# Kernel tuning notes

Hardware: AMD Instinct MI355X
Metric: run time of the kernel (lower is better)

## Reference

```python
import jax, jax.numpy as jnp
import numpy as np

N_NODES = 150000       # original nodes
N_FRAG_NODES = 300000  # nodes duplicated across fragments
N_FRAGS = 30000        # number of fragments (segments of fragments_batch)
E = 1200000            # edges in combined fragment graph
D = 128                # nhid


def seg_mean(x, seg, num):
    s = jax.ops.segment_sum(x, seg, num_segments=num)
    c = jax.ops.segment_sum(jnp.ones((x.shape[0], 1), x.dtype), seg, num_segments=num)
    return s / jnp.maximum(c, 1.0)


def setup_inputs() -> dict:
    key = jax.random.key(0)
    ks = jax.random.split(key, 8)
    x = jax.random.normal(ks[0], (N_NODES, D), dtype=jnp.float32)
    mapper = jax.random.randint(ks[1], (N_FRAG_NODES,), 0, N_NODES)
    batch = jnp.sort(jax.random.randint(ks[2], (N_FRAG_NODES,), 0, N_FRAGS))
    edge_index = jax.random.randint(ks[3], (2, E), 0, N_FRAG_NODES)
    W_u = jax.random.normal(ks[4], (D, D), dtype=jnp.float32) * 0.05
    b_u = jnp.zeros((D,), dtype=jnp.float32)
    W_gcn = jax.random.normal(ks[5], (D, D), dtype=jnp.float32) * 0.05
    b_gcn = jnp.zeros((D,), dtype=jnp.float32)
    return {
        "x": x,
        "fragments_nodes_mapper": mapper,
        "fragments_batch": batch,
        "edge_index": edge_index,
        "W_u": W_u,
        "b_u": b_u,
        "W_gcn": W_gcn,
        "b_gcn": b_gcn,
        "i": 0,
    }


def gcn_conv(x, edge_index, W, b, n):
    # PyG GCNConv: add self loops, symmetric normalization D^-1/2 (A+I) D^-1/2, then linear.
    xw = x @ W  # [n, D]
    loops = jnp.arange(n, dtype=edge_index.dtype)
    row = jnp.concatenate([edge_index[0], loops])  # source
    col = jnp.concatenate([edge_index[1], loops])  # target (aggregation index)
    deg = jax.ops.segment_sum(jnp.ones(row.shape[0], x.dtype), col, num_segments=n)
    dinv = jnp.where(deg > 0, jax.lax.rsqrt(jnp.maximum(deg, 1.0)), 0.0)
    norm = dinv[row] * dinv[col]  # [E+n]
    msg = xw[row] * norm[:, None]
    out = jax.ops.segment_sum(msg, col, num_segments=n)
    return out + b


def reference(x, fragments_nodes_mapper, fragments_batch, edge_index, W_u, b_u, W_gcn, b_gcn, i):
    if i == 0:
        x = x[fragments_nodes_mapper]  # gather: [N_FRAG_NODES, D]
    # fragment-level mean pooling, broadcast back to fragment-nodes
    fragment = seg_mean(x, fragments_batch, N_FRAGS)[fragments_batch]
    # U[i-1]: MLP(nhid, nhid, nlayer=1, with_final_activation=True) -> Linear + ReLU
    x = x + jax.nn.relu(fragment @ W_u + b_u)
    # pool duplicated fragment-nodes back onto original nodes, then re-broadcast
    x = seg_mean(x, fragments_nodes_mapper, N_NODES)[fragments_nodes_mapper]
    # GCN over the combined fragment graph
    x = gcn_conv(x, edge_index, W_gcn, b_gcn, N_FRAG_NODES)
    fragment_x = seg_mean(x, fragments_batch, N_FRAGS)  # [N_FRAGS, D]
    return (fragment_x, x)
```

## Files before the change

### kernel.cpp

```cpp
#include <hip/hip_runtime.h>
#include <hip/hip_bf16.h>

#define N_NODES      150000
#define N_FRAG_NODES 300000
#define N_FRAGS      30000
#define NEDGE        1200000
#define NCNT         (N_NODES + N_FRAG_NODES)
#define D            128
#define DV           32
#define SCAN_TILE    1024

typedef __attribute__((ext_vector_type(8))) short short8;
typedef __attribute__((ext_vector_type(8))) unsigned short u16x8;
typedef __attribute__((ext_vector_type(4))) float f32x4;
typedef __attribute__((ext_vector_type(2))) int i32x2;

__device__ __forceinline__ unsigned short f2bf(float f) {
    unsigned u = __float_as_uint(f);
    u = (u + 0x7FFFu + ((u >> 16) & 1u)) >> 16;
    return (unsigned short)u;
}
__device__ __forceinline__ float bf2f(unsigned short u) {
    return __uint_as_float((unsigned)u << 16);
}

__global__ void k_prep(const int* __restrict__ mapper, const int* __restrict__ batch,
                       const int* __restrict__ ecol, int* __restrict__ mcnt,
                       int* __restrict__ ccnt, int* __restrict__ startb) {
    int i = blockIdx.x * blockDim.x + threadIdx.x;
    if (i < NEDGE) atomicAdd(&ccnt[ecol[i]], 1);
    if (i < N_FRAG_NODES) atomicAdd(&mcnt[mapper[i]], 1);
    if (i <= N_FRAGS) {
        int lo = 0, hi = N_FRAG_NODES;
        while (lo < hi) { int mid = (lo + hi) >> 1; if (batch[mid] < i) lo = mid + 1; else hi = mid; }
        startb[i] = lo;
    }
}

__global__ void k_scan_tile(const int* __restrict__ cnt, int* __restrict__ combst,
                            int* __restrict__ tsum) {
    __shared__ int buf[SCAN_TILE];
    int tid = threadIdx.x;
    int i = blockIdx.x * SCAN_TILE + tid;
    int v = (i < NCNT) ? cnt[i] : 0;
    buf[tid] = v;
    __syncthreads();
    for (int off = 1; off < SCAN_TILE; off <<= 1) {
        int t = (tid >= off) ? buf[tid - off] : 0;
        __syncthreads();
        buf[tid] += t;
        __syncthreads();
    }
    if (i < NCNT) combst[i] = buf[tid] - v;
    if (tid == SCAN_TILE - 1) tsum[blockIdx.x] = buf[tid];
}

__global__ void k_scan_tsum(int* __restrict__ tsum, int ntiles,
                            int* __restrict__ mstart, int* __restrict__ cstart) {
    __shared__ int buf[SCAN_TILE];
    int tid = threadIdx.x;
    int v = (tid < ntiles) ? tsum[tid] : 0;
    buf[tid] = v;
    __syncthreads();
    for (int off = 1; off < SCAN_TILE; off <<= 1) {
        int t = (tid >= off) ? buf[tid - off] : 0;
        __syncthreads();
        buf[tid] += t;
        __syncthreads();
    }
    if (tid < ntiles) tsum[tid] = buf[tid] - v;
    if (tid == SCAN_TILE - 1) {
        mstart[N_NODES] = N_FRAG_NODES;
        cstart[N_FRAG_NODES] = buf[tid] - N_FRAG_NODES;
    }
}

__global__ void k_scan_add(const int* __restrict__ combst, const int* __restrict__ tsum,
                           int* __restrict__ mstart, int* __restrict__ cstart) {
    int i = blockIdx.x * blockDim.x + threadIdx.x;
    if (i >= NCNT) return;
    int v = combst[i] + tsum[i >> 10];
    if (i < N_NODES) mstart[i] = v;
    else cstart[i - N_NODES] = v - N_FRAG_NODES;
}

__global__ void k_frag_mean(const float4* __restrict__ x4, const int* __restrict__ mapper,
                            const int* __restrict__ startb, ushort4* __restrict__ frag16) {
    int g = threadIdx.x >> 5, lane = threadIdx.x & 31;
    int b = blockIdx.x * 8 + g;
    if (b >= N_FRAGS) return;
    int s = startb[b], e = startb[b + 1];
    float4 sA = {0.f, 0.f, 0.f, 0.f}, sB = {0.f, 0.f, 0.f, 0.f};
    int j = s;
    for (; j + 2 <= e; j += 2) {
        int m0 = mapper[j], m1 = mapper[j + 1];
        float4 v0 = x4[(size_t)m0 * DV + lane];
        float4 v1 = x4[(size_t)m1 * DV + lane];
        sA.x += v0.x; sA.y += v0.y; sA.z += v0.z; sA.w += v0.w;
        sB.x += v1.x; sB.y += v1.y; sB.z += v1.z; sB.w += v1.w;
    }
    if (j < e) {
        int m0 = mapper[j];
        float4 v0 = x4[(size_t)m0 * DV + lane];
        sA.x += v0.x; sA.y += v0.y; sA.z += v0.z; sA.w += v0.w;
    }
    float c = (float)(e - s); if (c < 1.f) c = 1.f;
    float inv = 1.f / c;
    ushort4 r = {f2bf((sA.x + sB.x) * inv), f2bf((sA.y + sB.y) * inv),
                 f2bf((sA.z + sB.z) * inv), f2bf((sA.w + sB.w) * inv)};
    frag16[(size_t)b * DV + lane] = r;
}

__global__ void k_build_wfrag(const float* __restrict__ W, short* __restrict__ wfrag) {
    int t = threadIdx.x;
    for (int e = t; e < 2048; e += 256) {
        int nt = e >> 8;
        int kk = (e >> 6) & 3;
        int lane = e & 63;
        int col = nt * 16 + (lane & 15);
        int kb = kk * 32 + ((lane >> 4) << 3);
        short8 v;
        #pragma unroll
        for (int j = 0; j < 8; ++j) v[j] = (short)f2bf(W[(kb + j) * D + col]);
        ((short8*)wfrag)[e] = v;
    }
}

template <bool RELU, bool BIAS>
__global__ void __launch_bounds__(256)
k_rowmat_mfma(const unsigned short* __restrict__ src16, const short* __restrict__ wfrag,
              const float* __restrict__ bias, unsigned short* __restrict__ dst16, int rows) {
    __shared__ short8 wl[2048];
    int tid = threadIdx.x;
    for (int e = tid; e < 2048; e += 256) wl[e] = ((const short8*)wfrag)[e];
    __syncthreads();
    int wv = tid >> 6, lane = tid & 63;
    int lrow = lane & 15;
    int lk8 = (lane >> 4);
    float bv[8];
    #pragma unroll
    for (int nt = 0; nt < 8; ++nt) bv[nt] = BIAS ? bias[nt * 16 + lrow] : 0.f;

    int chunk = blockIdx.x * 64;
    {
        int r = chunk + wv * 16 + lrow;
        short8 af[4];
        if (r < rows) {
            const short8* rowp = (const short8*)(src16 + (size_t)r * D);
            #pragma unroll
            for (int kk = 0; kk < 4; ++kk) af[kk] = rowp[kk * 4 + lk8];
        } else {
            #pragma unroll
            for (int kk = 0; kk < 4; ++kk) af[kk] = (short8)0;
        }
        f32x4 acc[8];
        #pragma unroll
        for (int nt = 0; nt < 8; ++nt) acc[nt] = (f32x4)0.f;
        #pragma unroll
        for (int nt = 0; nt < 8; ++nt) {
            #pragma unroll
            for (int kk = 0; kk < 4; ++kk)
                acc[nt] = __builtin_amdgcn_mfma_f32_16x16x32_bf16(
                              af[kk], wl[(nt * 4 + kk) * 64 + lane], acc[nt], 0, 0, 0);
        }
        int orow0 = chunk + wv * 16 + ((lane >> 4) << 2);
        #pragma unroll
        for (int nt = 0; nt < 8; ++nt) {
            int col = nt * 16 + lrow;
            #pragma unroll
            for (int reg = 0; reg < 4; ++reg) {
                int orow = orow0 + reg;
                if (orow < rows) {
                    float v = acc[nt][reg] + bv[nt];
                    if (RELU) v = fmaxf(v, 0.f);
                    dst16[(size_t)orow * D + col] = f2bf(v);
                }
            }
        }
    }
}

__global__ void k_sval(const int* __restrict__ mapper, const int* __restrict__ cstart,
                       int2* __restrict__ sval) {
    int r = blockIdx.x * blockDim.x + threadIdx.x;
    if (r >= N_FRAG_NODES) return;
    int2 v;
    v.x = mapper[r];
    v.y = __float_as_int(rsqrtf((float)(cstart[r + 1] - cstart[r] + 1)));
    sval[r] = v;
}

__global__ void k_fill(const int* __restrict__ mapper, const int* __restrict__ batch,
                       const int* __restrict__ erow, const int* __restrict__ ecol,
                       const int* __restrict__ mstart, int* __restrict__ mcnt,
                       int* __restrict__ mvals, const int* __restrict__ cstart,
                       int* __restrict__ ccnt, const int2* __restrict__ sval,
                       int2* __restrict__ erecs) {
    int i = blockIdx.x * blockDim.x + threadIdx.x;
    if (i < N_FRAG_NODES) {
        int k = mapper[i];
        int pos = atomicSub(&mcnt[k], 1) - 1;
        mvals[mstart[k] + pos] = batch[i];
    }
    if (i < NEDGE) {
        int c = ecol[i], r = erow[i];
        int pos = atomicSub(&ccnt[c], 1) - 1;
        erecs[cstart[c] + pos] = sval[r];
    }
}

__global__ void k_pool_csr(const float4* __restrict__ x4, const u16x8* __restrict__ fragu8,
                           const int* __restrict__ mstart, const int* __restrict__ mvals,
                           u16x8* __restrict__ pooled8) {
    int g = threadIdx.x >> 4, lane = threadIdx.x & 15;
    int n = blockIdx.x * 16 + g;
    if (n >= N_NODES) return;
    int s = mstart[n], e = mstart[n + 1];
    u16x8 out = (u16x8)0;
    if (e > s) {
        float accA[8], accB[8];
        #pragma unroll
        for (int j = 0; j < 8; ++j) { accA[j] = 0.f; accB[j] = 0.f; }
        int t = s;
        for (; t + 2 <= e; t += 2) {
            int b0 = mvals[t], b1 = mvals[t + 1];
            u16x8 u0 = fragu8[(size_t)b0 * 16 + lane];
            u16x8 u1 = fragu8[(size_t)b1 * 16 + lane];
            #pragma unroll
            for (int j = 0; j < 8; ++j) {
                accA[j] += bf2f(u0[j]);
                accB[j] += bf2f(u1[j]);
            }
        }
        if (t < e) {
            int b0 = mvals[t];
            u16x8 u0 = fragu8[(size_t)b0 * 16 + lane];
            #pragma unroll
            for (int j = 0; j < 8; ++j) accA[j] += bf2f(u0[j]);
        }
        float inv = 1.f / (float)(e - s);
        float4 xv0 = x4[(size_t)n * DV + lane * 2];
        float4 xv1 = x4[(size_t)n * DV + lane * 2 + 1];
        out[0] = f2bf(fmaf(accA[0] + accB[0], inv, xv0.x));
        out[1] = f2bf(fmaf(accA[1] + accB[1], inv, xv0.y));
        out[2] = f2bf(fmaf(accA[2] + accB[2], inv, xv0.z));
        out[3] = f2bf(fmaf(accA[3] + accB[3], inv, xv0.w));
        out[4] = f2bf(fmaf(accA[4] + accB[4], inv, xv1.x));
        out[5] = f2bf(fmaf(accA[5] + accB[5], inv, xv1.y));
        out[6] = f2bf(fmaf(accA[6] + accB[6], inv, xv1.z));
        out[7] = f2bf(fmaf(accA[7] + accB[7], inv, xv1.w));
    }
    pooled8[(size_t)n * 16 + lane] = out;
}

__global__ void k_gcn_frag(const int* __restrict__ startb, const int* __restrict__ cstart,
                           const int2* __restrict__ sval, const i32x2* __restrict__ erecs,
                           const u16x8* __restrict__ pw8, const float* __restrict__ bgcn,
                           f32x4* __restrict__ xout4, float4* __restrict__ fout4) {
    int g = threadIdx.x >> 4, lane = threadIdx.x & 15;
    int b = blockIdx.x * 16 + g;
    if (b >= N_FRAGS) return;
    int js = startb[b], je = startb[b + 1];
    const float4* bg4 = (const float4*)bgcn;
    float4 bgA = bg4[lane * 2], bgB = bg4[lane * 2 + 1];
    float mA[8];
    #pragma unroll
    for (int j = 0; j < 8; ++j) mA[j] = 0.f;
    for (int c = js; c < je; ++c) {
        int s = cstart[c], e = cstart[c + 1];
        int2 sv = sval[c];
        float dc = __int_as_float(sv.y);
        float accA[8], accB[8];
        #pragma unroll
        for (int j = 0; j < 8; ++j) { accA[j] = 0.f; accB[j] = 0.f; }
        int t = s;
        for (; t + 2 <= e; t += 2) {
            i32x2 r0 = __builtin_nontemporal_load(&erecs[t]);
            i32x2 r1 = __builtin_nontemporal_load(&erecs[t + 1]);
            u16x8 u0 = pw8[(size_t)r0.x * 16 + lane];
            u16x8 u1 = pw8[(size_t)r1.x * 16 + lane];
            float w0 = __int_as_float(r0.y), w1 = __int_as_float(r1.y);
            #pragma unroll
            for (int j = 0; j < 8; ++j) {
                accA[j] = fmaf(bf2f(u0[j]), w0, accA[j]);
                accB[j] = fmaf(bf2f(u1[j]), w1, accB[j]);
            }
        }
        if (t < e) {
            i32x2 r0 = __builtin_nontemporal_load(&erecs[t]);
            u16x8 u0 = pw8[(size_t)r0.x * 16 + lane];
            float w0 = __int_as_float(r0.y);
            #pragma unroll
            for (int j = 0; j < 8; ++j) accA[j] = fmaf(bf2f(u0[j]), w0, accA[j]);
        }
        u16x8 su = pw8[(size_t)sv.x * 16 + lane];
        float dc2 = dc * dc;
        float o[8];
        #pragma unroll
        for (int j = 0; j < 8; ++j) {
            o[j] = fmaf(accA[j] + accB[j], dc, bf2f(su[j]) * dc2);
            mA[j] += o[j];
        }
        f32x4 o0 = {o[0] + bgA.x, o[1] + bgA.y, o[2] + bgA.z, o[3] + bgA.w};
        f32x4 o1 = {o[4] + bgB.x, o[5] + bgB.y, o[6] + bgB.z, o[7] + bgB.w};
        __builtin_nontemporal_store(o0, &xout4[(size_t)c * DV + lane * 2]);
        __builtin_nontemporal_store(o1, &xout4[(size_t)c * DV + lane * 2 + 1]);
    }
    float4 r0 = {0.f, 0.f, 0.f, 0.f}, r1 = {0.f, 0.f, 0.f, 0.f};
    if (je > js) {
        float inv = 1.f / (float)(je - js);
        r0.x = fmaf(mA[0], inv, bgA.x); r0.y = fmaf(mA[1], inv, bgA.y);
        r0.z = fmaf(mA[2], inv, bgA.z); r0.w = fmaf(mA[3], inv, bgA.w);
        r1.x = fmaf(mA[4], inv, bgB.x); r1.y = fmaf(mA[5], inv, bgB.y);
        r1.z = fmaf(mA[6], inv, bgB.z); r1.w = fmaf(mA[7], inv, bgB.w);
    }
    fout4[(size_t)b * DV + lane * 2] = r0;
    fout4[(size_t)b * DV + lane * 2 + 1] = r1;
}

extern "C" void kernel_launch(void* const* d_in, const int* in_sizes, int n_in,
                              void* d_out, int out_size, void* d_ws, size_t ws_size,
                              hipStream_t stream) {
    const float* x      = (const float*)d_in[0];
    const int*   mapper = (const int*)d_in[1];
    const int*   batch  = (const int*)d_in[2];
    const int*   erow   = (const int*)d_in[3];
    const int*   ecol   = erow + NEDGE;
    const float* W_u    = (const float*)d_in[4];
    const float* b_u    = (const float*)d_in[5];
    const float* W_gcn  = (const float*)d_in[6];
    const float* b_gcn  = (const float*)d_in[7];

    float* fout = (float*)d_out;
    float* xout = fout + (size_t)N_FRAGS * D;

    short*  wfragU   = (short*)d_ws;
    short*  wfragG   = wfragU + 16384;
    int2*   erecs    = (int2*)(wfragG + 16384);
    int2*   sval     = erecs + NEDGE;
    unsigned short* frag16   = (unsigned short*)(sval + N_FRAG_NODES);
    unsigned short* pooled16 = frag16 + (size_t)N_FRAGS * D;
    int*    startb = (int*)(pooled16 + (size_t)N_NODES * D);
    int*    mstart = startb + (N_FRAGS + 1);
    int*    cstart = mstart + (N_NODES + 1);
    int*    mcnt   = cstart + (N_FRAG_NODES + 1);
    int*    ccnt   = mcnt + N_NODES;
    int*    mvals  = ccnt + N_FRAG_NODES;
    int*    combst = mvals + N_FRAG_NODES;
    int*    tsum   = combst + NCNT;

    hipMemsetAsync(mcnt, 0, (size_t)NCNT * sizeof(int), stream);

    k_build_wfrag<<<1, 256, 0, stream>>>(W_u, wfragU);
    k_build_wfrag<<<1, 256, 0, stream>>>(W_gcn, wfragG);

    k_prep<<<(NEDGE + 255) / 256, 256, 0, stream>>>(mapper, batch, ecol, mcnt, ccnt, startb);

    int ntiles = (NCNT + SCAN_TILE - 1) / SCAN_TILE;
    k_scan_tile<<<ntiles, SCAN_TILE, 0, stream>>>(mcnt, combst, tsum);
    k_scan_tsum<<<1, SCAN_TILE, 0, stream>>>(tsum, ntiles, mstart, cstart);
    k_scan_add<<<(NCNT + 255) / 256, 256, 0, stream>>>(combst, tsum, mstart, cstart);

    k_frag_mean<<<(N_FRAGS + 7) / 8, 256, 0, stream>>>((const float4*)x, mapper, startb,
                                                       (ushort4*)frag16);
    k_rowmat_mfma<true, true><<<(N_FRAGS + 63) / 64, 256, 0, stream>>>(
        frag16, wfragU, b_u, frag16, N_FRAGS);

    k_sval<<<(N_FRAG_NODES + 255) / 256, 256, 0, stream>>>(mapper, cstart, sval);
    k_fill<<<(NEDGE + 255) / 256, 256, 0, stream>>>(mapper, batch, erow, ecol,
                                                    mstart, mcnt, mvals,
                                                    cstart, ccnt, sval, erecs);

    k_pool_csr<<<(N_NODES + 15) / 16, 256, 0, stream>>>((const float4*)x, (const u16x8*)frag16,
                                                        mstart, mvals, (u16x8*)pooled16);
    k_rowmat_mfma<false, false><<<(N_NODES + 63) / 64, 256, 0, stream>>>(
        pooled16, wfragG, nullptr, pooled16, N_NODES);

    k_gcn_frag<<<(N_FRAGS + 15) / 16, 256, 0, stream>>>(startb, cstart, sval, (const i32x2*)erecs,
                                                        (const u16x8*)pooled16, b_gcn,
                                                        (f32x4*)xout, (float4*)fout);
}
```

Baseline: 386.5 us.

## Split GCN gather per node and compute fragment means in separate kernel

The fused per-fragment GCN kernel, where each 16-lane group walked every node of a fragment in turn, is replaced by a per-node gather kernel with one 16-lane group per fragment-node and a 4-way unrolled edge loop. A second kernel then reads the written fp32 node outputs back and averages them per fragment. This spreads the work over many more groups and evens out load imbalance between fragments. The cost is an extra launch and a re-read of the 300k x 128 fp32 output, which the nontemporal stores may keep out of cache.

```diff
diff --git a/kernel.cpp b/kernel.cpp
--- a/kernel.cpp
+++ b/kernel.cpp
@@ -253,69 +253,84 @@
     pooled8[(size_t)n * 16 + lane] = out;
 }
 
-__global__ void k_gcn_frag(const int* __restrict__ startb, const int* __restrict__ cstart,
-                           const int2* __restrict__ sval, const i32x2* __restrict__ erecs,
-                           const u16x8* __restrict__ pw8, const float* __restrict__ bgcn,
-                           f32x4* __restrict__ xout4, float4* __restrict__ fout4) {
+__global__ void k_gcn_gather(const int* __restrict__ cstart, const int2* __restrict__ sval,
+                             const i32x2* __restrict__ erecs, const u16x8* __restrict__ pw8,
+                             const float* __restrict__ bgcn, f32x4* __restrict__ xout4) {
     int g = threadIdx.x >> 4, lane = threadIdx.x & 15;
-    int b = blockIdx.x * 16 + g;
+    int c = blockIdx.x * 16 + g;
+    if (c >= N_FRAG_NODES) return;
+    int s = cstart[c], e = cstart[c + 1];
+    int2 sv = sval[c];
+    float dc = __int_as_float(sv.y);
+    float acc0[8], acc1[8], acc2[8], acc3[8];
+    #pragma unroll
+    for (int j = 0; j < 8; ++j) { acc0[j] = 0.f; acc1[j] = 0.f; acc2[j] = 0.f; acc3[j] = 0.f; }
+    int t = s;
+    for (; t + 4 <= e; t += 4) {
+        i32x2 r0 = __builtin_nontemporal_load(&erecs[t]);
+        i32x2 r1 = __builtin_nontemporal_load(&erecs[t + 1]);
+        i32x2 r2 = __builtin_nontemporal_load(&erecs[t + 2]);
+        i32x2 r3 = __builtin_nontemporal_load(&erecs[t + 3]);
+        u16x8 u0 = pw8[(size_t)r0.x * 16 + lane];
+        u16x8 u1 = pw8[(size_t)r1.x * 16 + lane];
+        u16x8 u2 = pw8[(size_t)r2.x * 16 + lane];
+        u16x8 u3 = pw8[(size_t)r3.x * 16 + lane];
+        float w0 = __int_as_float(r0.y), w1 = __int_as_float(r1.y);
+        float w2 = __int_as_float(r2.y), w3 = __int_as_float(r3.y);
+        #pragma unroll
+        for (int j = 0; j < 8; ++j) {
+            acc0[j] = fmaf(bf2f(u0[j]), w0, acc0[j]);
+            acc1[j] = fmaf(bf2f(u1[j]), w1, acc1[j]);
+            acc2[j] = fmaf(bf2f(u2[j]), w2, acc2[j]);
+            acc3[j] = fmaf(bf2f(u3[j]), w3, acc3[j]);
+        }
+    }
+    for (; t < e; ++t) {
+        i32x2 r0 = __builtin_nontemporal_load(&erecs[t]);
+        u16x8 u0 = pw8[(size_t)r0.x * 16 + lane];
+        float w0 = __int_as_float(r0.y);
+        #pragma unroll
+        for (int j = 0; j < 8; ++j) acc0[j] = fmaf(bf2f(u0[j]), w0, acc0[j]);
+    }
+    u16x8 su = pw8[(size_t)sv.x * 16 + lane];
+    float dc2 = dc * dc;
+    const float4* bg4 = (const float4*)bgcn;
+    float4 b0 = bg4[lane * 2], b1 = bg4[lane * 2 + 1];
+    float o[8];
+    #pragma unroll
+    for (int j = 0; j < 8; ++j)
+        o[j] = fmaf((acc0[j] + acc1[j]) + (acc2[j] + acc3[j]), dc, bf2f(su[j]) * dc2);
+    f32x4 o0 = {o[0] + b0.x, o[1] + b0.y, o[2] + b0.z, o[3] + b0.w};
+    f32x4 o1 = {o[4] + b1.x, o[5] + b1.y, o[6] + b1.z, o[7] + b1.w};
+    __builtin_nontemporal_store(o0, &xout4[(size_t)c * DV + lane * 2]);
+    __builtin_nontemporal_store(o1, &xout4[(size_t)c * DV + lane * 2 + 1]);
+}
+
+__global__ void k_frag_x(const float4* __restrict__ x4, const int* __restrict__ startb,
+                         float4* __restrict__ fout4) {
+    int g = threadIdx.x >> 5, lane = threadIdx.x & 31;
+    int b = blockIdx.x * 8 + g;
     if (b >= N_FRAGS) return;
-    int js = startb[b], je = startb[b + 1];
-    const float4* bg4 = (const float4*)bgcn;
-    float4 bgA = bg4[lane * 2], bgB = bg4[lane * 2 + 1];
-    float mA[8];
-    #pragma unroll
-    for (int j = 0; j < 8; ++j) mA[j] = 0.f;
-    for (int c = js; c < je; ++c) {
-        int s = cstart[c], e = cstart[c + 1];
-        int2 sv = sval[c];
-        float dc = __int_as_float(sv.y);
-        float accA[8], accB[8];
-        #pragma unroll
-        for (int j = 0; j < 8; ++j) { accA[j] = 0.f; accB[j] = 0.f; }
-        int t = s;
-        for (; t + 2 <= e; t += 2) {
-            i32x2 r0 = __builtin_nontemporal_load(&erecs[t]);
-            i32x2 r1 = __builtin_nontemporal_load(&erecs[t + 1]);
-            u16x8 u0 = pw8[(size_t)r0.x * 16 + lane];
-            u16x8 u1 = pw8[(size_t)r1.x * 16 + lane];
-            float w0 = __int_as_float(r0.y), w1 = __int_as_float(r1.y);
-            #pragma unroll
-            for (int j = 0; j < 8; ++j) {
-                accA[j] = fmaf(bf2f(u0[j]), w0, accA[j]);
-                accB[j] = fmaf(bf2f(u1[j]), w1, accB[j]);
-            }
-        }
-        if (t < e) {
-            i32x2 r0 = __builtin_nontemporal_load(&erecs[t]);
-            u16x8 u0 = pw8[(size_t)r0.x * 16 + lane];
-            float w0 = __int_as_float(r0.y);
-            #pragma unroll
-            for (int j = 0; j < 8; ++j) accA[j] = fmaf(bf2f(u0[j]), w0, accA[j]);
-        }
-        u16x8 su = pw8[(size_t)sv.x * 16 + lane];
-        float dc2 = dc * dc;
-        float o[8];
-        #pragma unroll
-        for (int j = 0; j < 8; ++j) {
-            o[j] = fmaf(accA[j] + accB[j], dc, bf2f(su[j]) * dc2);
-            mA[j] += o[j];
-        }
-        f32x4 o0 = {o[0] + bgA.x, o[1] + bgA.y, o[2] + bgA.z, o[3] + bgA.w};
-        f32x4 o1 = {o[4] + bgB.x, o[5] + bgB.y, o[6] + bgB.z, o[7] + bgB.w};
-        __builtin_nontemporal_store(o0, &xout4[(size_t)c * DV + lane * 2]);
-        __builtin_nontemporal_store(o1, &xout4[(size_t)c * DV + lane * 2 + 1]);
-    }
-    float4 r0 = {0.f, 0.f, 0.f, 0.f}, r1 = {0.f, 0.f, 0.f, 0.f};
-    if (je > js) {
-        float inv = 1.f / (float)(je - js);
-        r0.x = fmaf(mA[0], inv, bgA.x); r0.y = fmaf(mA[1], inv, bgA.y);
-        r0.z = fmaf(mA[2], inv, bgA.z); r0.w = fmaf(mA[3], inv, bgA.w);
-        r1.x = fmaf(mA[4], inv, bgB.x); r1.y = fmaf(mA[5], inv, bgB.y);
-        r1.z = fmaf(mA[6], inv, bgB.z); r1.w = fmaf(mA[7], inv, bgB.w);
-    }
-    fout4[(size_t)b * DV + lane * 2] = r0;
-    fout4[(size_t)b * DV + lane * 2 + 1] = r1;
+    int s = startb[b], e = startb[b + 1];
+    float4 sA = {0.f, 0.f, 0.f, 0.f}, sB = {0.f, 0.f, 0.f, 0.f};
+    int j = s;
+    for (; j + 2 <= e; j += 2) {
+        float4 v0 = x4[(size_t)j * DV + lane];
+        float4 v1 = x4[(size_t)(j + 1) * DV + lane];
+        sA.x += v0.x; sA.y += v0.y; sA.z += v0.z; sA.w += v0.w;
+        sB.x += v1.x; sB.y += v1.y; sB.z += v1.z; sB.w += v1.w;
+    }
+    if (j < e) {
+        float4 v0 = x4[(size_t)j * DV + lane];
+        sA.x += v0.x; sA.y += v0.y; sA.z += v0.z; sA.w += v0.w;
+    }
+    float4 r = {0.f, 0.f, 0.f, 0.f};
+    if (e > s) {
+        float inv = 1.f / (float)(e - s);
+        r.x = (sA.x + sB.x) * inv; r.y = (sA.y + sB.y) * inv;
+        r.z = (sA.z + sB.z) * inv; r.w = (sA.w + sB.w) * inv;
+    }
+    fout4[(size_t)b * DV + lane] = r;
 }
 
 extern "C" void kernel_launch(void* const* d_in, const int* in_sizes, int n_in,
@@ -376,7 +391,8 @@
     k_rowmat_mfma<false, false><<<(N_NODES + 63) / 64, 256, 0, stream>>>(
         pooled16, wfragG, nullptr, pooled16, N_NODES);
 
-    k_gcn_frag<<<(N_FRAGS + 15) / 16, 256, 0, stream>>>(startb, cstart, sval, (const i32x2*)erecs,
-                                                        (const u16x8*)pooled16, b_gcn,
-                                                        (f32x4*)xout, (float4*)fout);
-}
+    k_gcn_gather<<<(N_FRAG_NODES + 15) / 16, 256, 0, stream>>>(cstart, sval, (const i32x2*)erecs,
+                                                               (const u16x8*)pooled16,
+                                                               b_gcn, (f32x4*)xout);
+    k_frag_x<<<(N_FRAGS + 7) / 8, 256, 0, stream>>>((const float4*)xout, startb, (float4*)fout);
+}
```

Measured after the change: 373.5 us. -3.4%, faster.
